# Optimization experiments

Hardware: AMD Instinct MI355X
Metric: run time of the kernel (lower is better)

The kernel has to match this reference:

```python
import jax, jax.numpy as jnp
import numpy as np
jax.config.update("jax_enable_x64", True)  # original does softmax in torch.double

B, H, S, D = 1, 16, 2048, 128

def setup_inputs() -> dict:
    key = jax.random.key(0)
    kq, kk, kv = jax.random.split(key, 3)
    return {
        "query_states": jax.random.normal(kq, (B, H, S, D), dtype=jnp.float32),
        "key_states": jax.random.normal(kk, (B, H, S, D), dtype=jnp.float32),
        "value_states": jax.random.normal(kv, (B, H, S, D), dtype=jnp.float32),
        "attention_mask": jnp.zeros((1, 1, S, S), dtype=jnp.float32),  # accepted but unused by the module
        "attention_dropout": 0,  # p=0.0 -> dropout is identity
    }

def reference(query_states, key_states, value_states, attention_mask, attention_dropout):
    head_dim = query_states.shape[-1]
    q_len = query_states.shape[-2]
    kv_len = key_states.shape[-2]
    # scores: [B,H,q,kv]
    attn = jnp.einsum("bhqd,bhkd->bhqk", query_states, key_states) / jnp.sqrt(
        jnp.asarray(head_dim, query_states.dtype))
    # causal mask: triu(ones, diagonal=1) -> mask strictly-future positions with -10000
    causal = jnp.triu(jnp.ones((q_len, kv_len), dtype=bool), k=1)
    attn = jnp.where(causal[None, None], jnp.asarray(-10000.0, attn.dtype), attn)
    # softmax in float64 (torch.double) then cast back, matching the original
    attn = jax.nn.softmax(attn.astype(jnp.float64), axis=-1).astype(query_states.dtype)
    # dropout p == attention_dropout == 0.0 -> no-op
    return jnp.einsum("bhqk,bhkd->bhqd", attn, value_states)
```

## Files before the change

kernel.cpp:

```cpp
#include <hip/hip_runtime.h>


#define NH  16
#define SEQ 2048
#define DIM 128
#define NT  64
#define SCALE 0.08838834764831845f

typedef __attribute__((ext_vector_type(8))) short    bf16x8;
typedef __attribute__((ext_vector_type(4))) float    f32x4;
typedef __attribute__((ext_vector_type(8))) unsigned short ushort8;

__device__ __forceinline__ unsigned short f2bf(float f) {
    unsigned u = __builtin_bit_cast(unsigned, f);
    u += 0x7FFFu + ((u >> 16) & 1u);
    return (unsigned short)(u >> 16);
}

__global__ void cvtq_kernel(const float* __restrict__ in, unsigned short* __restrict__ out) {
    const float SC = SCALE * 1.4426950408889634f;
    const int i = blockIdx.x * blockDim.x + threadIdx.x;
    const float4* p = reinterpret_cast<const float4*>(in) + (size_t)i * 2;
    const float4 a = p[0], b = p[1];
    ushort8 o;
    o[0]=f2bf(a.x*SC); o[1]=f2bf(a.y*SC); o[2]=f2bf(a.z*SC); o[3]=f2bf(a.w*SC);
    o[4]=f2bf(b.x*SC); o[5]=f2bf(b.y*SC); o[6]=f2bf(b.z*SC); o[7]=f2bf(b.w*SC);
    reinterpret_cast<ushort8*>(out)[i] = o;
}

__global__ void kp_kernel(const float* __restrict__ K, unsigned short* __restrict__ Kp) {
    __shared__ float sm[32][133];
    const int t = blockIdx.x, head = blockIdx.y, tid = threadIdx.x;
    const size_t base = (size_t)head * SEQ * DIM + (size_t)t * 32 * DIM;
#pragma unroll
    for (int i = 0; i < 16; ++i) {
        const int idx = i * 256 + tid;
        sm[idx >> 7][idx & 127] = K[base + idx];
    }
    __syncthreads();
    ushort8* outp = reinterpret_cast<ushort8*>(Kp) + (size_t)(head * NT + t) * 512;
#pragma unroll
    for (int c = tid; c < 512; c += 256) {
        const int j = c >> 6, lane = c & 63, l15 = lane & 15, lg = lane >> 4;
        const int kl = (j >> 2) * 16 + l15, d0 = (j & 3) * 32 + lg * 8;
        ushort8 o;
#pragma unroll
        for (int e = 0; e < 8; ++e) o[e] = f2bf(sm[kl][d0 + e]);
        outp[c] = o;
    }
}

__global__ void vp_kernel(const float* __restrict__ V, unsigned short* __restrict__ Vp) {
    __shared__ float sm[32][133];
    const int t = blockIdx.x, head = blockIdx.y, tid = threadIdx.x;
    const size_t base = (size_t)head * SEQ * DIM + (size_t)t * 32 * DIM;
#pragma unroll
    for (int i = 0; i < 16; ++i) {
        const int idx = i * 256 + tid;
        sm[idx >> 7][idx & 127] = V[base + idx];
    }
    __syncthreads();
    ushort8* outp = reinterpret_cast<ushort8*>(Vp) + (size_t)(head * NT + t) * 512;
#pragma unroll
    for (int c = tid; c < 512; c += 256) {
        const int db = c >> 6, lane = c & 63, l15 = lane & 15, lg = lane >> 4;
        const int d = db * 16 + l15;
        ushort8 o;
#pragma unroll
        for (int e = 0; e < 4; ++e) o[e]     = f2bf(sm[lg * 4 + e][d]);
#pragma unroll
        for (int e = 0; e < 4; ++e) o[4 + e] = f2bf(sm[16 + lg * 4 + e][d]);
        outp[c] = o;
    }
}

__global__ __launch_bounds__(256, 2) void attn_main(
    const unsigned short* __restrict__ Qb, const unsigned short* __restrict__ Kp,
    const unsigned short* __restrict__ Vp, float* __restrict__ O)
{
    const int lane = threadIdx.x & 63;
    const int wid  = threadIdx.x >> 6;
    const int l15  = lane & 15;
    const int lg   = lane >> 4;
    const int head = blockIdx.y;
    const int qt   = gridDim.x - 1 - blockIdx.x;
    const int qbase = qt * 64 + wid * 16;
    const int nt    = qbase / 32 + 1;
    const size_t ho = (size_t)head * SEQ * DIM;

    bf16x8 qfrag[4];
    {
        const unsigned short* qrow = Qb + ho + (size_t)(qbase + l15) * DIM;
#pragma unroll
        for (int mi = 0; mi < 4; ++mi)
            qfrag[mi] = *reinterpret_cast<const bf16x8*>(qrow + mi * 32 + lg * 8);
    }

    f32x4 oacc[8];
#pragma unroll
    for (int i = 0; i < 8; ++i) oacc[i] = f32x4{0.f, 0.f, 0.f, 0.f};
    float l_run = 0.f;

    const bf16x8* kbase = reinterpret_cast<const bf16x8*>(Kp) + (size_t)head * NT * 512 + lane;
    const bf16x8* vbase = reinterpret_cast<const bf16x8*>(Vp) + (size_t)head * NT * 512 + lane;

    for (int t = 0; t < nt; ++t) {
        const int kb = t * 32;
        const bf16x8* kp = kbase + (size_t)t * 512;
        const bf16x8* vp = vbase + (size_t)t * 512;

        bf16x8 kf[8], vf[8];
#pragma unroll
        for (int j = 0; j < 8; ++j) kf[j] = kp[j * 64];
#pragma unroll
        for (int j = 0; j < 8; ++j) vf[j] = vp[j * 64];

        f32x4 sT0 = f32x4{0.f,0.f,0.f,0.f}, sT1 = f32x4{0.f,0.f,0.f,0.f};
#pragma unroll
        for (int mi = 0; mi < 4; ++mi) {
            sT0 = __builtin_amdgcn_mfma_f32_16x16x32_bf16(kf[mi],     qfrag[mi], sT0, 0, 0, 0);
            sT1 = __builtin_amdgcn_mfma_f32_16x16x32_bf16(kf[4 + mi], qfrag[mi], sT1, 0, 0, 0);
        }

        float s[8];
#pragma unroll
        for (int r = 0; r < 4; ++r) { s[r] = sT0[r]; s[4 + r] = sT1[r]; }
        if (kb + 31 > qbase) {
            const int qg = qbase + l15;
#pragma unroll
            for (int r = 0; r < 4; ++r) {
                if (kb + lg * 4 + r > qg)      s[r]     = -1e30f;
                if (kb + 16 + lg * 4 + r > qg) s[4 + r] = -1e30f;
            }
        }

        float p[8];
#pragma unroll
        for (int i = 0; i < 8; ++i) { p[i] = exp2f(s[i]); l_run += p[i]; }
        bf16x8 pf;
#pragma unroll
        for (int i = 0; i < 8; ++i) pf[i] = (short)f2bf(p[i]);

#pragma unroll
        for (int db = 0; db < 8; ++db)
            oacc[db] = __builtin_amdgcn_mfma_f32_16x16x32_bf16(vf[db], pf, oacc[db], 0, 0, 0);
    }

    float lsum = l_run;
    lsum += __shfl_xor(lsum, 16);
    lsum += __shfl_xor(lsum, 32);
    const float inv = 1.f / lsum;
    float* orow = O + ho + (size_t)(qbase + l15) * DIM;
#pragma unroll
    for (int db = 0; db < 8; ++db) {
        const float4 o{oacc[db][0] * inv, oacc[db][1] * inv, oacc[db][2] * inv, oacc[db][3] * inv};
        *reinterpret_cast<float4*>(orow + db * 16 + lg * 4) = o;
    }
}

__global__ __launch_bounds__(256, 2) void attn_fb(
    const float* __restrict__ Qf, const float* __restrict__ Kf, const float* __restrict__ Vf,
    float* __restrict__ O)
{
    const int lane = threadIdx.x & 63;
    const int wid  = threadIdx.x >> 6;
    const int l15  = lane & 15;
    const int lg   = lane >> 4;
    const int head = blockIdx.y;
    const int qt   = gridDim.x - 1 - blockIdx.x;
    const int qbase = qt * 64 + wid * 16;
    const int qmax  = qbase + 15;
    const size_t ho = (size_t)head * SEQ * DIM;

    bf16x8 qfrag[4];
    const float* qrow = Qf + ho + (size_t)(qbase + l15) * DIM;
#pragma unroll
    for (int mi = 0; mi < 4; ++mi) {
        const float4 a = *reinterpret_cast<const float4*>(qrow + mi * 32 + lg * 8);
        const float4 b = *reinterpret_cast<const float4*>(qrow + mi * 32 + lg * 8 + 4);
        bf16x8 f;
        f[0]=(short)f2bf(a.x); f[1]=(short)f2bf(a.y); f[2]=(short)f2bf(a.z); f[3]=(short)f2bf(a.w);
        f[4]=(short)f2bf(b.x); f[5]=(short)f2bf(b.y); f[6]=(short)f2bf(b.z); f[7]=(short)f2bf(b.w);
        qfrag[mi] = f;
    }
    f32x4 oacc[8];
#pragma unroll
    for (int i = 0; i < 8; ++i) oacc[i] = f32x4{0.f, 0.f, 0.f, 0.f};
    float m_run = -1e38f, l_run = 0.f;
    for (int kb = 0; kb <= qmax; kb += 32) {
        f32x4 sT0 = f32x4{0.f,0.f,0.f,0.f}, sT1 = f32x4{0.f,0.f,0.f,0.f};
        const float* k0 = Kf + ho + (size_t)(kb + l15) * DIM;
        const float* k1 = k0 + 16 * DIM;
#pragma unroll
        for (int mi = 0; mi < 4; ++mi) {
            float4 a = *reinterpret_cast<const float4*>(k0 + mi * 32 + lg * 8);
            float4 b = *reinterpret_cast<const float4*>(k0 + mi * 32 + lg * 8 + 4);
            bf16x8 f;
            f[0]=(short)f2bf(a.x); f[1]=(short)f2bf(a.y); f[2]=(short)f2bf(a.z); f[3]=(short)f2bf(a.w);
            f[4]=(short)f2bf(b.x); f[5]=(short)f2bf(b.y); f[6]=(short)f2bf(b.z); f[7]=(short)f2bf(b.w);
            sT0 = __builtin_amdgcn_mfma_f32_16x16x32_bf16(f, qfrag[mi], sT0, 0, 0, 0);
            a = *reinterpret_cast<const float4*>(k1 + mi * 32 + lg * 8);
            b = *reinterpret_cast<const float4*>(k1 + mi * 32 + lg * 8 + 4);
            f[0]=(short)f2bf(a.x); f[1]=(short)f2bf(a.y); f[2]=(short)f2bf(a.z); f[3]=(short)f2bf(a.w);
            f[4]=(short)f2bf(b.x); f[5]=(short)f2bf(b.y); f[6]=(short)f2bf(b.z); f[7]=(short)f2bf(b.w);
            sT1 = __builtin_amdgcn_mfma_f32_16x16x32_bf16(f, qfrag[mi], sT1, 0, 0, 0);
        }
        float s[8];
#pragma unroll
        for (int r = 0; r < 4; ++r) { s[r] = sT0[r] * SCALE; s[4 + r] = sT1[r] * SCALE; }
        if (kb + 31 > qbase) {
            const int qg = qbase + l15;
#pragma unroll
            for (int r = 0; r < 4; ++r) {
                if (kb + lg * 4 + r > qg)      s[r]     = -1e30f;
                if (kb + 16 + lg * 4 + r > qg) s[4 + r] = -1e30f;
            }
        }
        float mt = s[0];
#pragma unroll
        for (int i = 1; i < 8; ++i) mt = fmaxf(mt, s[i]);
        mt = fmaxf(mt, __shfl_xor(mt, 16));
        mt = fmaxf(mt, __shfl_xor(mt, 32));
        const float m_new = fmaxf(m_run, mt);
        const float alpha = __expf(m_run - m_new);
        float p[8], psum = 0.f;
#pragma unroll
        for (int i = 0; i < 8; ++i) { p[i] = __expf(s[i] - m_new); psum += p[i]; }
        psum += __shfl_xor(psum, 16);
        psum += __shfl_xor(psum, 32);
        l_run = l_run * alpha + psum;
        m_run = m_new;
#pragma unroll
        for (int i = 0; i < 8; ++i) {
            oacc[i][0] *= alpha; oacc[i][1] *= alpha; oacc[i][2] *= alpha; oacc[i][3] *= alpha;
        }
        bf16x8 pf;
#pragma unroll
        for (int i = 0; i < 8; ++i) pf[i] = (short)f2bf(p[i]);
#pragma unroll
        for (int db = 0; db < 8; ++db) {
            bf16x8 vf;
#pragma unroll
            for (int e = 0; e < 8; ++e) {
                const int key = kb + 16 * (e >> 2) + lg * 4 + (e & 3);
                vf[e] = (short)f2bf(Vf[ho + (size_t)key * DIM + db * 16 + l15]);
            }
            oacc[db] = __builtin_amdgcn_mfma_f32_16x16x32_bf16(vf, pf, oacc[db], 0, 0, 0);
        }
    }
    const float inv = 1.f / l_run;
    float* orow = O + ho + (size_t)(qbase + l15) * DIM;
#pragma unroll
    for (int db = 0; db < 8; ++db) {
        const float4 o{oacc[db][0] * inv, oacc[db][1] * inv, oacc[db][2] * inv, oacc[db][3] * inv};
        *reinterpret_cast<float4*>(orow + db * 16 + lg * 4) = o;
    }
}

extern "C" void kernel_launch(void* const* d_in, const int* in_sizes, int n_in,
                              void* d_out, int out_size, void* d_ws, size_t ws_size,
                              hipStream_t stream) {
    const float* Q = (const float*)d_in[0];
    const float* K = (const float*)d_in[1];
    const float* V = (const float*)d_in[2];
    float* O = (float*)d_out;

    const size_t ELEMS = (size_t)NH * SEQ * DIM;
    const size_t NEED  = 3 * ELEMS * sizeof(unsigned short);

    if (ws_size >= NEED) {
        unsigned short* Qb = (unsigned short*)d_ws;
        unsigned short* Kp = Qb + ELEMS;
        unsigned short* Vp = Kp + ELEMS;
        cvtq_kernel<<<dim3(ELEMS / 8 / 256), dim3(256), 0, stream>>>(Q, Qb);
        kp_kernel<<<dim3(NT, NH), dim3(256), 0, stream>>>(K, Kp);
        vp_kernel<<<dim3(NT, NH), dim3(256), 0, stream>>>(V, Vp);
        attn_main<<<dim3(SEQ / 64, NH), dim3(256), 0, stream>>>(Qb, Kp, Vp, O);
    } else {
        attn_fb<<<dim3(SEQ / 64, NH), dim3(256), 0, stream>>>(Q, K, V, O);
    }
}
```

Measured before the change: 172.8 us.

## Fuse Q conversion into attention, merge K/V packing, balance causal work, double-buffer loads

Drops the separate Q conversion kernel: the attention kernel now reads fp32 Q, scales it and converts it to bf16 in registers. The K and V packing kernels are merged into one launch that uses blockIdx.z to choose K or V. The attention grid becomes 16x16 blocks of 512 threads, where each block pairs light and heavy causal query tiles so every block does a similar amount of work. K/V tile loads are double-buffered to overlap with MFMA compute, at the cost of more registers under launch_bounds(512,2).

```diff
diff --git a/kernel.cpp b/kernel.cpp
--- a/kernel.cpp
+++ b/kernel.cpp
@@ -6,6 +6,7 @@
 #define DIM 128
 #define NT  64
 #define SCALE 0.08838834764831845f
+#define SCLOG2E 0.12751364605544427f
 
 typedef __attribute__((ext_vector_type(8))) short    bf16x8;
 typedef __attribute__((ext_vector_type(4))) float    f32x4;
@@ -17,65 +18,47 @@
     return (unsigned short)(u >> 16);
 }
 
-__global__ void cvtq_kernel(const float* __restrict__ in, unsigned short* __restrict__ out) {
-    const float SC = SCALE * 1.4426950408889634f;
-    const int i = blockIdx.x * blockDim.x + threadIdx.x;
-    const float4* p = reinterpret_cast<const float4*>(in) + (size_t)i * 2;
-    const float4 a = p[0], b = p[1];
-    ushort8 o;
-    o[0]=f2bf(a.x*SC); o[1]=f2bf(a.y*SC); o[2]=f2bf(a.z*SC); o[3]=f2bf(a.w*SC);
-    o[4]=f2bf(b.x*SC); o[5]=f2bf(b.y*SC); o[6]=f2bf(b.z*SC); o[7]=f2bf(b.w*SC);
-    reinterpret_cast<ushort8*>(out)[i] = o;
-}
-
-__global__ void kp_kernel(const float* __restrict__ K, unsigned short* __restrict__ Kp) {
+__global__ void pack_kv(const float* __restrict__ K, const float* __restrict__ V,
+                        unsigned short* __restrict__ Kp, unsigned short* __restrict__ Vp) {
     __shared__ float sm[32][133];
     const int t = blockIdx.x, head = blockIdx.y, tid = threadIdx.x;
+    const float* __restrict__ src = blockIdx.z ? V : K;
     const size_t base = (size_t)head * SEQ * DIM + (size_t)t * 32 * DIM;
 #pragma unroll
     for (int i = 0; i < 16; ++i) {
         const int idx = i * 256 + tid;
-        sm[idx >> 7][idx & 127] = K[base + idx];
+        sm[idx >> 7][idx & 127] = src[base + idx];
     }
     __syncthreads();
-    ushort8* outp = reinterpret_cast<ushort8*>(Kp) + (size_t)(head * NT + t) * 512;
-#pragma unroll
-    for (int c = tid; c < 512; c += 256) {
-        const int j = c >> 6, lane = c & 63, l15 = lane & 15, lg = lane >> 4;
-        const int kl = (j >> 2) * 16 + l15, d0 = (j & 3) * 32 + lg * 8;
-        ushort8 o;
-#pragma unroll
-        for (int e = 0; e < 8; ++e) o[e] = f2bf(sm[kl][d0 + e]);
-        outp[c] = o;
-    }
-}
-
-__global__ void vp_kernel(const float* __restrict__ V, unsigned short* __restrict__ Vp) {
-    __shared__ float sm[32][133];
-    const int t = blockIdx.x, head = blockIdx.y, tid = threadIdx.x;
-    const size_t base = (size_t)head * SEQ * DIM + (size_t)t * 32 * DIM;
-#pragma unroll
-    for (int i = 0; i < 16; ++i) {
-        const int idx = i * 256 + tid;
-        sm[idx >> 7][idx & 127] = V[base + idx];
-    }
-    __syncthreads();
-    ushort8* outp = reinterpret_cast<ushort8*>(Vp) + (size_t)(head * NT + t) * 512;
-#pragma unroll
-    for (int c = tid; c < 512; c += 256) {
-        const int db = c >> 6, lane = c & 63, l15 = lane & 15, lg = lane >> 4;
-        const int d = db * 16 + l15;
-        ushort8 o;
-#pragma unroll
-        for (int e = 0; e < 4; ++e) o[e]     = f2bf(sm[lg * 4 + e][d]);
-#pragma unroll
-        for (int e = 0; e < 4; ++e) o[4 + e] = f2bf(sm[16 + lg * 4 + e][d]);
-        outp[c] = o;
-    }
-}
-
-__global__ __launch_bounds__(256, 2) void attn_main(
-    const unsigned short* __restrict__ Qb, const unsigned short* __restrict__ Kp,
+    if (blockIdx.z == 0) {
+        ushort8* outp = reinterpret_cast<ushort8*>(Kp) + (size_t)(head * NT + t) * 512;
+#pragma unroll
+        for (int c = tid; c < 512; c += 256) {
+            const int j = c >> 6, lane = c & 63, l15 = lane & 15, lg = lane >> 4;
+            const int kl = (j >> 2) * 16 + l15, d0 = (j & 3) * 32 + lg * 8;
+            ushort8 o;
+#pragma unroll
+            for (int e = 0; e < 8; ++e) o[e] = f2bf(sm[kl][d0 + e]);
+            outp[c] = o;
+        }
+    } else {
+        ushort8* outp = reinterpret_cast<ushort8*>(Vp) + (size_t)(head * NT + t) * 512;
+#pragma unroll
+        for (int c = tid; c < 512; c += 256) {
+            const int db = c >> 6, lane = c & 63, l15 = lane & 15, lg = lane >> 4;
+            const int d = db * 16 + l15;
+            ushort8 o;
+#pragma unroll
+            for (int e = 0; e < 4; ++e) o[e]     = f2bf(sm[lg * 4 + e][d]);
+#pragma unroll
+            for (int e = 0; e < 4; ++e) o[4 + e] = f2bf(sm[16 + lg * 4 + e][d]);
+            outp[c] = o;
+        }
+    }
+}
+
+__global__ __launch_bounds__(512, 2) void attn_main(
+    const float* __restrict__ Qf, const unsigned short* __restrict__ Kp,
     const unsigned short* __restrict__ Vp, float* __restrict__ O)
 {
     const int lane = threadIdx.x & 63;
@@ -83,17 +66,27 @@
     const int l15  = lane & 15;
     const int lg   = lane >> 4;
     const int head = blockIdx.y;
-    const int qt   = gridDim.x - 1 - blockIdx.x;
-    const int qbase = qt * 64 + wid * 16;
-    const int nt    = qbase / 32 + 1;
+    const int s4   = wid & 3;
+    const int lightIdx = blockIdx.x * 4 + s4;
+    const int qtile = (wid < 4) ? lightIdx : (127 - lightIdx);
+    const int qbase = qtile * 16;
+    const int nt    = qtile / 2 + 1;
     const size_t ho = (size_t)head * SEQ * DIM;
 
     bf16x8 qfrag[4];
     {
-        const unsigned short* qrow = Qb + ho + (size_t)(qbase + l15) * DIM;
-#pragma unroll
-        for (int mi = 0; mi < 4; ++mi)
-            qfrag[mi] = *reinterpret_cast<const bf16x8*>(qrow + mi * 32 + lg * 8);
+        const float* qrow = Qf + ho + (size_t)(qbase + l15) * DIM;
+#pragma unroll
+        for (int mi = 0; mi < 4; ++mi) {
+            const float4 a = *reinterpret_cast<const float4*>(qrow + mi * 32 + lg * 8);
+            const float4 b = *reinterpret_cast<const float4*>(qrow + mi * 32 + lg * 8 + 4);
+            bf16x8 f;
+            f[0]=(short)f2bf(a.x*SCLOG2E); f[1]=(short)f2bf(a.y*SCLOG2E);
+            f[2]=(short)f2bf(a.z*SCLOG2E); f[3]=(short)f2bf(a.w*SCLOG2E);
+            f[4]=(short)f2bf(b.x*SCLOG2E); f[5]=(short)f2bf(b.y*SCLOG2E);
+            f[6]=(short)f2bf(b.z*SCLOG2E); f[7]=(short)f2bf(b.w*SCLOG2E);
+            qfrag[mi] = f;
+        }
     }
 
     f32x4 oacc[8];
@@ -104,46 +97,53 @@
     const bf16x8* kbase = reinterpret_cast<const bf16x8*>(Kp) + (size_t)head * NT * 512 + lane;
     const bf16x8* vbase = reinterpret_cast<const bf16x8*>(Vp) + (size_t)head * NT * 512 + lane;
 
-    for (int t = 0; t < nt; ++t) {
-        const int kb = t * 32;
-        const bf16x8* kp = kbase + (size_t)t * 512;
-        const bf16x8* vp = vbase + (size_t)t * 512;
-
-        bf16x8 kf[8], vf[8];
-#pragma unroll
-        for (int j = 0; j < 8; ++j) kf[j] = kp[j * 64];
-#pragma unroll
-        for (int j = 0; j < 8; ++j) vf[j] = vp[j * 64];
-
+    auto LOADT = [&](int T, bf16x8 (&KF)[8], bf16x8 (&VF)[8]) {
+        const bf16x8* kp = kbase + (size_t)T * 512;
+        const bf16x8* vp = vbase + (size_t)T * 512;
+#pragma unroll
+        for (int j = 0; j < 8; ++j) KF[j] = kp[j * 64];
+#pragma unroll
+        for (int j = 0; j < 8; ++j) VF[j] = vp[j * 64];
+    };
+    auto COMPUTE = [&](int T, bf16x8 (&KF)[8], bf16x8 (&VF)[8]) {
         f32x4 sT0 = f32x4{0.f,0.f,0.f,0.f}, sT1 = f32x4{0.f,0.f,0.f,0.f};
 #pragma unroll
         for (int mi = 0; mi < 4; ++mi) {
-            sT0 = __builtin_amdgcn_mfma_f32_16x16x32_bf16(kf[mi],     qfrag[mi], sT0, 0, 0, 0);
-            sT1 = __builtin_amdgcn_mfma_f32_16x16x32_bf16(kf[4 + mi], qfrag[mi], sT1, 0, 0, 0);
-        }
-
-        float s[8];
-#pragma unroll
-        for (int r = 0; r < 4; ++r) { s[r] = sT0[r]; s[4 + r] = sT1[r]; }
+            sT0 = __builtin_amdgcn_mfma_f32_16x16x32_bf16(KF[mi],     qfrag[mi], sT0, 0, 0, 0);
+            sT1 = __builtin_amdgcn_mfma_f32_16x16x32_bf16(KF[4 + mi], qfrag[mi], sT1, 0, 0, 0);
+        }
+        float sc[8];
+#pragma unroll
+        for (int r = 0; r < 4; ++r) { sc[r] = sT0[r]; sc[4 + r] = sT1[r]; }
+        const int kb = T * 32;
         if (kb + 31 > qbase) {
             const int qg = qbase + l15;
 #pragma unroll
             for (int r = 0; r < 4; ++r) {
-                if (kb + lg * 4 + r > qg)      s[r]     = -1e30f;
-                if (kb + 16 + lg * 4 + r > qg) s[4 + r] = -1e30f;
+                if (kb + lg * 4 + r > qg)      sc[r]     = -1e30f;
+                if (kb + 16 + lg * 4 + r > qg) sc[4 + r] = -1e30f;
             }
         }
-
         float p[8];
 #pragma unroll
-        for (int i = 0; i < 8; ++i) { p[i] = exp2f(s[i]); l_run += p[i]; }
+        for (int i = 0; i < 8; ++i) { p[i] = exp2f(sc[i]); l_run += p[i]; }
         bf16x8 pf;
 #pragma unroll
         for (int i = 0; i < 8; ++i) pf[i] = (short)f2bf(p[i]);
-
 #pragma unroll
         for (int db = 0; db < 8; ++db)
-            oacc[db] = __builtin_amdgcn_mfma_f32_16x16x32_bf16(vf[db], pf, oacc[db], 0, 0, 0);
+            oacc[db] = __builtin_amdgcn_mfma_f32_16x16x32_bf16(VF[db], pf, oacc[db], 0, 0, 0);
+    };
+
+    bf16x8 kA[8], vA[8], kB[8], vB[8];
+    LOADT(0, kA, vA);
+    for (int t = 0; t < nt; ) {
+        if (t + 1 < nt) LOADT(t + 1, kB, vB);
+        COMPUTE(t, kA, vA);
+        ++t; if (t >= nt) break;
+        if (t + 1 < nt) LOADT(t + 1, kA, vA);
+        COMPUTE(t, kB, vB);
+        ++t;
     }
 
     float lsum = l_run;
@@ -266,16 +266,13 @@
     float* O = (float*)d_out;
 
     const size_t ELEMS = (size_t)NH * SEQ * DIM;
-    const size_t NEED  = 3 * ELEMS * sizeof(unsigned short);
+    const size_t NEED  = 2 * ELEMS * sizeof(unsigned short);
 
     if (ws_size >= NEED) {
-        unsigned short* Qb = (unsigned short*)d_ws;
-        unsigned short* Kp = Qb + ELEMS;
+        unsigned short* Kp = (unsigned short*)d_ws;
         unsigned short* Vp = Kp + ELEMS;
-        cvtq_kernel<<<dim3(ELEMS / 8 / 256), dim3(256), 0, stream>>>(Q, Qb);
-        kp_kernel<<<dim3(NT, NH), dim3(256), 0, stream>>>(K, Kp);
-        vp_kernel<<<dim3(NT, NH), dim3(256), 0, stream>>>(V, Vp);
-        attn_main<<<dim3(SEQ / 64, NH), dim3(256), 0, stream>>>(Qb, Kp, Vp, O);
+        pack_kv<<<dim3(NT, NH, 2), dim3(256), 0, stream>>>(K, V, Kp, Vp);
+        attn_main<<<dim3(16, NH), dim3(512), 0, stream>>>(Q, Kp, Vp, O);
     } else {
         attn_fb<<<dim3(SEQ / 64, NH), dim3(256), 0, stream>>>(Q, K, V, O);
     }
```

New measurement: 148.6 us. 1.16x faster.
